# Optimization experiments

Hardware: AMD Instinct MI355X
Metric: run time of the kernel (lower is better)

The kernel has to match this reference:

```python
import jax, jax.numpy as jnp
import numpy as np

N_TOKEN = 267735
HEAD = 20000
CUTOFFS = [20000, 20008, 20016, 200000, 267735]  # from cl_root_leaf_dict with 2 roots of 8 leaves
N_ROOTS = 2


def setup_inputs() -> dict:
    key = jax.random.key(0)
    k1, k2, k3, k4 = jax.random.split(key, 4)
    N, D = 1024, 1024
    hidden = jax.random.normal(k1, (N, D), dtype=jnp.float32)
    target = jax.random.randint(k2, (N,), 0, N_TOKEN)
    W = jax.random.normal(k3, (N_TOKEN, D), dtype=jnp.float32) * 0.02
    b = jnp.zeros((N_TOKEN,), dtype=jnp.float32)
    cluster_weight = jax.random.normal(k4, (2, D), dtype=jnp.float32) * 0.02
    cluster_bias = jnp.zeros((2,), dtype=jnp.float32)
    return {"hidden": hidden, "target": target, "W": W, "b": b,
            "cluster_weight": cluster_weight, "cluster_bias": cluster_bias}


def _nll(hidden, target, W, b, cw, cb):
    cutoff_ends = [0] + CUTOFFS
    # head = first 20000 vocab rows + 2 cluster rows (d_proj == d_embed -> no projection)
    head_w = jnp.concatenate([W[:HEAD], cw], axis=0)          # [20002, D]
    head_b = jnp.concatenate([b[:HEAD], cb], axis=0)          # [20002]
    head_lp = jax.nn.log_softmax(hidden @ head_w.T + head_b, axis=-1)  # [N, 20002]
    n_head_cols = head_lp.shape[1]
    rows = jnp.arange(hidden.shape[0])
    # segment 0: target in [0, 20000) -> nll directly from head log-probs
    lp0 = head_lp[rows, jnp.clip(target, 0, HEAD - 1)]
    nll = -lp0  # only valid where target < HEAD; overwritten below otherwise
    for i in range(1, len(CUTOFFS)):
        l, r = cutoff_ends[i], cutoff_ends[i + 1]
        # per-segment tail logits for all tokens (masked combine keeps shapes static)
        tail_lp = jax.nn.log_softmax(hidden @ W[l:r].T + b[l:r], axis=-1)  # [N, r-l]
        # routing column exactly as in the torch code:
        # j = i-1 for root segments, -(i - n_roots) for the two cluster segments
        j = (i - 1) if i <= N_ROOTS else (n_head_cols - (i - N_ROOTS))
        lp_i = head_lp[:, j] + tail_lp[rows, jnp.clip(target - l, 0, r - l - 1)]
        mask = (target >= l) & (target < r)
        nll = jnp.where(mask, -lp_i, nll)
    return nll


def reference(hidden, target, W, b, cluster_weight, cluster_bias):
    return _nll(hidden, target, W, b, cluster_weight, cluster_bias)
```

## Files before the change

kernel.cpp:

```cpp
#include <hip/hip_runtime.h>
#include <hip/hip_bf16.h>

#define D_DIM 1024
#define NTOK 267735
#define NEXT_ 267737
#define HEADN 20000

typedef __attribute__((ext_vector_type(8))) short bf16x8;
typedef __attribute__((ext_vector_type(4))) float f32x4;

__device__ __forceinline__ int seg_of(int c){
  if (c < HEADN)  return 0;
  if (c < 20008)  return 1;
  if (c < 20016)  return 2;
  if (c < 200000) return 3;
  if (c < NTOK)   return 4;
  return 0;
}

__device__ __forceinline__ unsigned pack2(float x, float y){
  __hip_bfloat16 a = __float2bfloat16(x);
  __hip_bfloat16 b = __float2bfloat16(y);
  unsigned short ua = *reinterpret_cast<unsigned short*>(&a);
  unsigned short ub = *reinterpret_cast<unsigned short*>(&b);
  return (unsigned)ua | ((unsigned)ub << 16);
}

#define BM 256
#define BN 128
#define BK 32
#define LDP 40
#define NTHREADS 512

__global__ __launch_bounds__(NTHREADS, 1) void gemm_lse_kernel(
    const float* __restrict__ hidden, const float* __restrict__ W,
    const float* __restrict__ bias,   const float* __restrict__ cw,
    const float* __restrict__ cb,     float* __restrict__ accg)
{
  __shared__ unsigned short lsA[BM * LDP];
  __shared__ unsigned short lsB[BN * LDP];

  const int tid = threadIdx.x;
  const int rowBase = blockIdx.x * BM;
  const int colBase = blockIdx.y * BN;

  const float* aSrc[4]; int aRow[4], aK4[4];
#pragma unroll
  for (int i=0;i<4;++i){
    int idx = tid + NTHREADS*i;
    aRow[i] = idx >> 3; aK4[i] = idx & 7;
    aSrc[i] = hidden + (size_t)(rowBase + aRow[i]) * D_DIM + aK4[i]*4;
  }
  const float* bSrc[2]; int bRow[2], bK4[2];
#pragma unroll
  for (int i=0;i<2;++i){
    int idx = tid + NTHREADS*i;
    bRow[i] = idx >> 3; bK4[i] = idx & 7;
    int c = colBase + bRow[i];
    const float* base;
    if (c < NTOK)       base = W  + (size_t)c * D_DIM;
    else if (c < NEXT_) base = cw + (size_t)(c - NTOK) * D_DIM;
    else                base = W;
    bSrc[i] = base + bK4[i]*4;
  }

  const int lane = tid & 63;
  const int wv = tid >> 6;
  const int wm = wv >> 1;
  const int wn = wv & 1;

  f32x4 acc[4][4];
#pragma unroll
  for (int i=0;i<4;++i)
#pragma unroll
    for (int j=0;j<4;++j) acc[i][j] = (f32x4){0.f,0.f,0.f,0.f};

  const int aRd = (wm*64 + (lane&15)) * LDP + (lane>>4)*8;
  const int bRd = (wn*64 + (lane&15)) * LDP + (lane>>4)*8;

  for (int kt = 0; kt < D_DIM/BK; ++kt){
    float4 av[4], bv[2];
#pragma unroll
    for (int i=0;i<4;++i) av[i] = *reinterpret_cast<const float4*>(aSrc[i] + kt*BK);
#pragma unroll
    for (int i=0;i<2;++i) bv[i] = *reinterpret_cast<const float4*>(bSrc[i] + kt*BK);
    __syncthreads();
#pragma unroll
    for (int i=0;i<4;++i){
      unsigned* p = reinterpret_cast<unsigned*>(&lsA[aRow[i]*LDP + aK4[i]*4]);
      p[0] = pack2(av[i].x, av[i].y); p[1] = pack2(av[i].z, av[i].w);
    }
#pragma unroll
    for (int i=0;i<2;++i){
      unsigned* p = reinterpret_cast<unsigned*>(&lsB[bRow[i]*LDP + bK4[i]*4]);
      p[0] = pack2(bv[i].x, bv[i].y); p[1] = pack2(bv[i].z, bv[i].w);
    }
    __syncthreads();
    bf16x8 afr[4], bfr[4];
#pragma unroll
    for (int f=0; f<4; ++f) afr[f] = *reinterpret_cast<const bf16x8*>(&lsA[aRd + f*16*LDP]);
#pragma unroll
    for (int f=0; f<4; ++f) bfr[f] = *reinterpret_cast<const bf16x8*>(&lsB[bRd + f*16*LDP]);
#pragma unroll
    for (int i=0;i<4;++i)
#pragma unroll
      for (int j=0;j<4;++j)
        acc[i][j] = __builtin_amdgcn_mfma_f32_16x16x32_bf16(afr[i], bfr[j], acc[i][j], 0, 0, 0);
  }

  int sq[4]; float bq[4];
#pragma unroll
  for (int f=0; f<4; ++f){
    int c = colBase + wn*64 + f*16 + (lane & 15);
    if (c < NTOK)       { sq[f] = seg_of(c); bq[f] = bias[c]; }
    else if (c < NEXT_) { sq[f] = 0;         bq[f] = cb[c - NTOK]; }
    else                { sq[f] = -1;        bq[f] = 0.f; }
  }
  int sfirst = seg_of(colBase);
  int clast  = colBase + BN - 1; if (clast > NEXT_-1) clast = NEXT_-1;
  int slast  = seg_of(clast);
  int smin = sfirst, smax = slast;
  if (slast < sfirst){ smin = 0; smax = 4; }

#pragma unroll
  for (int i=0;i<4;++i){
#pragma unroll
    for (int r=0;r<4;++r){
      float e[4];
#pragma unroll
      for (int f=0;f<4;++f) e[f] = __expf(acc[i][f][r] + bq[f]);
      int rowg = rowBase + wm*64 + i*16 + (lane>>4)*4 + r;
      for (int s = smin; s <= smax; ++s){
        float p = 0.f;
#pragma unroll
        for (int f=0;f<4;++f) p += (sq[f]==s) ? e[f] : 0.f;
#pragma unroll
        for (int off=1; off<16; off<<=1) p += __shfl_xor(p, off, 16);
        if ((lane & 15) == 0 && p != 0.f) atomicAdd(&accg[rowg*8 + s], p);
      }
    }
  }
}

__global__ __launch_bounds__(256) void finalize_kernel(
    const float* __restrict__ hidden, const int* __restrict__ target,
    const float* __restrict__ W,      const float* __restrict__ bias,
    const float* __restrict__ cw,     const float* __restrict__ cb,
    const float* __restrict__ accg,   float* __restrict__ out)
{
  const int row  = blockIdx.x * 4 + (threadIdx.x >> 6);
  const int lane = threadIdx.x & 63;
  const int t = target[row];

  const float4* h4 = reinterpret_cast<const float4*>(hidden + (size_t)row * D_DIM);
  const float4* w1 = reinterpret_cast<const float4*>(W + (size_t)t * D_DIM);
  int s = 0; const float* jraw = W; float jb = 0.f;
  if (t >= HEADN){
    if      (t < 20008)  { s=1; jraw = W;          jb = bias[0]; }
    else if (t < 20016)  { s=2; jraw = W + D_DIM;  jb = bias[1]; }
    else if (t < 200000) { s=3; jraw = cw + D_DIM; jb = cb[1];   }
    else                 { s=4; jraw = cw;         jb = cb[0];   }
  }
  const float4* w2 = reinterpret_cast<const float4*>(jraw);

  float p1 = 0.f, p2 = 0.f;
#pragma unroll
  for (int j=0;j<4;++j){
    float4 hv = h4[lane + 64*j];
    float4 av = w1[lane + 64*j];
    float4 bv = w2[lane + 64*j];
    p1 += hv.x*av.x + hv.y*av.y + hv.z*av.z + hv.w*av.w;
    p2 += hv.x*bv.x + hv.y*bv.y + hv.z*bv.z + hv.w*bv.w;
  }
#pragma unroll
  for (int off=32; off; off>>=1){
    p1 += __shfl_xor(p1, off, 64);
    p2 += __shfl_xor(p2, off, 64);
  }

  if (lane == 0){
    float lseH = __logf(accg[row*8 + 0]);
    float nll;
    if (t < HEADN){
      nll = -(p1 + bias[t] - lseH);
    } else {
      float lseS = __logf(accg[row*8 + s]);
      nll = -((p2 + jb - lseH) + (p1 + bias[t] - lseS));
    }
    out[row] = nll;
  }
}

extern "C" void kernel_launch(void* const* d_in, const int* in_sizes, int n_in,
                              void* d_out, int out_size, void* d_ws, size_t ws_size,
                              hipStream_t stream)
{
  const float* hidden = (const float*)d_in[0];
  const int*   target = (const int*)  d_in[1];
  const float* W      = (const float*)d_in[2];
  const float* bias   = (const float*)d_in[3];
  const float* cw     = (const float*)d_in[4];
  const float* cb     = (const float*)d_in[5];
  float* out  = (float*)d_out;
  float* accg = (float*)d_ws;

  hipMemsetAsync(accg, 0, 1024*8*sizeof(float), stream);

  dim3 grid(1024/BM, (NEXT_ + BN - 1)/BN);
  gemm_lse_kernel<<<grid, NTHREADS, 0, stream>>>(hidden, W, bias, cw, cb, accg);
  finalize_kernel<<<256, 256, 0, stream>>>(hidden, target, W, bias, cw, cb, accg, out);
}
```

Baseline: 1.012 ms.

## Sort rows by target segment and skip unneeded tail GEMM tiles

A new prep kernel buckets the rows by the segment their target falls in, builds a permutation and per-segment row ranges, and zeroes the accumulators in place of the memset. The GEMM kernel reads hidden rows through this permutation and returns early for column tiles whose tail segment has no rows in the current row block, since those tail logsumexps are never used. It also replaces padded LDS rows with an XOR swizzle and prefetches the next k-slice into registers to overlap global loads with the MFMA work. The cost is an extra tiny single-block kernel launch and an indirect row gather.

Result: slower. 1.711 ms (+69.1%).

```diff
diff --git a/kernel.cpp b/kernel.cpp
--- a/kernel.cpp
+++ b/kernel.cpp
@@ -29,27 +29,72 @@
 #define BM 256
 #define BN 128
 #define BK 32
-#define LDP 40
 #define NTHREADS 512
+
+__global__ void prep_kernel(const int* __restrict__ target,
+                            float* __restrict__ accg,
+                            int* __restrict__ perm, int* __restrict__ segB)
+{
+  __shared__ int cnt[5]; __shared__ int base[5];
+  int t = threadIdx.x;
+  if (t < 5) cnt[t] = 0;
+  __syncthreads();
+  for (int i=0;i<8;++i) accg[t*8+i] = 0.f;
+  int s = seg_of(target[t]);
+  int pos = atomicAdd(&cnt[s], 1);
+  __syncthreads();
+  if (t == 0){
+    int acc = 0;
+    for (int q=0;q<5;++q){ base[q]=acc; segB[q*2]=acc; acc+=cnt[q]; segB[q*2+1]=acc; }
+  }
+  __syncthreads();
+  perm[base[s] + pos] = t;
+}
+
+__device__ __forceinline__ int swz_w(int r, int k4){
+  int c = (k4 >> 1) ^ ((r >> 1) & 3);
+  return r*32 + c*8 + (k4 & 1)*4;
+}
+__device__ __forceinline__ int swz_r(int row, int q){
+  return row*32 + ((q ^ ((row >> 1) & 3)) << 3);
+}
 
 __global__ __launch_bounds__(NTHREADS, 1) void gemm_lse_kernel(
     const float* __restrict__ hidden, const float* __restrict__ W,
     const float* __restrict__ bias,   const float* __restrict__ cw,
-    const float* __restrict__ cb,     float* __restrict__ accg)
-{
-  __shared__ unsigned short lsA[BM * LDP];
-  __shared__ unsigned short lsB[BN * LDP];
-
+    const float* __restrict__ cb,     float* __restrict__ accg,
+    const int* __restrict__ perm,     const int* __restrict__ segB)
+{
   const int tid = threadIdx.x;
   const int rowBase = blockIdx.x * BM;
   const int colBase = blockIdx.y * BN;
 
+  {
+    int cfirst = colBase;
+    int clast  = colBase + BN - 1; if (clast > NEXT_-1) clast = NEXT_-1;
+    bool need = (clast >= NTOK);
+    int clast2 = clast < NTOK ? clast : NTOK-1;
+    int sf = seg_of(cfirst), sl = seg_of(clast2);
+    for (int s = sf; s <= sl; ++s){
+      if (s == 0) { need = true; break; }
+      if (segB[2*s] < rowBase + BM && segB[2*s+1] > rowBase) need = true;
+    }
+    if (!need) return;
+  }
+
+  __shared__ unsigned short lsA[BM * 32];
+  __shared__ unsigned short lsB[BN * 32];
+  __shared__ int pperm[BM];
+
+  if (tid < BM) pperm[tid] = perm[rowBase + tid];
+  __syncthreads();
+
   const float* aSrc[4]; int aRow[4], aK4[4];
 #pragma unroll
   for (int i=0;i<4;++i){
     int idx = tid + NTHREADS*i;
     aRow[i] = idx >> 3; aK4[i] = idx & 7;
-    aSrc[i] = hidden + (size_t)(rowBase + aRow[i]) * D_DIM + aK4[i]*4;
+    aSrc[i] = hidden + (size_t)pperm[aRow[i]] * D_DIM + aK4[i]*4;
   }
   const float* bSrc[2]; int bRow[2], bK4[2];
 #pragma unroll
@@ -68,6 +113,8 @@
   const int wv = tid >> 6;
   const int wm = wv >> 1;
   const int wn = wv & 1;
+  const int q  = lane >> 4;
+  const int r16 = lane & 15;
 
   f32x4 acc[4][4];
 #pragma unroll
@@ -75,32 +122,36 @@
 #pragma unroll
     for (int j=0;j<4;++j) acc[i][j] = (f32x4){0.f,0.f,0.f,0.f};
 
-  const int aRd = (wm*64 + (lane&15)) * LDP + (lane>>4)*8;
-  const int bRd = (wn*64 + (lane&15)) * LDP + (lane>>4)*8;
+  float4 av[4], bv[2];
+#pragma unroll
+  for (int i=0;i<4;++i) av[i] = *reinterpret_cast<const float4*>(aSrc[i]);
+#pragma unroll
+  for (int i=0;i<2;++i) bv[i] = *reinterpret_cast<const float4*>(bSrc[i]);
 
   for (int kt = 0; kt < D_DIM/BK; ++kt){
-    float4 av[4], bv[2];
-#pragma unroll
-    for (int i=0;i<4;++i) av[i] = *reinterpret_cast<const float4*>(aSrc[i] + kt*BK);
-#pragma unroll
-    for (int i=0;i<2;++i) bv[i] = *reinterpret_cast<const float4*>(bSrc[i] + kt*BK);
     __syncthreads();
 #pragma unroll
     for (int i=0;i<4;++i){
-      unsigned* p = reinterpret_cast<unsigned*>(&lsA[aRow[i]*LDP + aK4[i]*4]);
+      unsigned* p = reinterpret_cast<unsigned*>(&lsA[swz_w(aRow[i], aK4[i])]);
       p[0] = pack2(av[i].x, av[i].y); p[1] = pack2(av[i].z, av[i].w);
     }
 #pragma unroll
     for (int i=0;i<2;++i){
-      unsigned* p = reinterpret_cast<unsigned*>(&lsB[bRow[i]*LDP + bK4[i]*4]);
+      unsigned* p = reinterpret_cast<unsigned*>(&lsB[swz_w(bRow[i], bK4[i])]);
       p[0] = pack2(bv[i].x, bv[i].y); p[1] = pack2(bv[i].z, bv[i].w);
     }
     __syncthreads();
+    if (kt + 1 < D_DIM/BK){
+#pragma unroll
+      for (int i=0;i<4;++i) av[i] = *reinterpret_cast<const float4*>(aSrc[i] + (kt+1)*BK);
+#pragma unroll
+      for (int i=0;i<2;++i) bv[i] = *reinterpret_cast<const float4*>(bSrc[i] + (kt+1)*BK);
+    }
     bf16x8 afr[4], bfr[4];
 #pragma unroll
-    for (int f=0; f<4; ++f) afr[f] = *reinterpret_cast<const bf16x8*>(&lsA[aRd + f*16*LDP]);
-#pragma unroll
-    for (int f=0; f<4; ++f) bfr[f] = *reinterpret_cast<const bf16x8*>(&lsB[bRd + f*16*LDP]);
+    for (int f=0; f<4; ++f) afr[f] = *reinterpret_cast<const bf16x8*>(&lsA[swz_r(wm*64 + f*16 + r16, q)]);
+#pragma unroll
+    for (int f=0; f<4; ++f) bfr[f] = *reinterpret_cast<const bf16x8*>(&lsB[swz_r(wn*64 + f*16 + r16, q)]);
 #pragma unroll
     for (int i=0;i<4;++i)
 #pragma unroll
@@ -111,7 +162,7 @@
   int sq[4]; float bq[4];
 #pragma unroll
   for (int f=0; f<4; ++f){
-    int c = colBase + wn*64 + f*16 + (lane & 15);
+    int c = colBase + wn*64 + f*16 + r16;
     if (c < NTOK)       { sq[f] = seg_of(c); bq[f] = bias[c]; }
     else if (c < NEXT_) { sq[f] = 0;         bq[f] = cb[c - NTOK]; }
     else                { sq[f] = -1;        bq[f] = 0.f; }
@@ -129,7 +180,7 @@
       float e[4];
 #pragma unroll
       for (int f=0;f<4;++f) e[f] = __expf(acc[i][f][r] + bq[f]);
-      int rowg = rowBase + wm*64 + i*16 + (lane>>4)*4 + r;
+      int rowg = pperm[wm*64 + i*16 + (lane>>4)*4 + r];
       for (int s = smin; s <= smax; ++s){
         float p = 0.f;
 #pragma unroll
@@ -203,10 +254,12 @@
   const float* cb     = (const float*)d_in[5];
   float* out  = (float*)d_out;
   float* accg = (float*)d_ws;
-
-  hipMemsetAsync(accg, 0, 1024*8*sizeof(float), stream);
+  int*   perm = (int*)((char*)d_ws + 32768);
+  int*   segB = (int*)((char*)d_ws + 36864);
+
+  prep_kernel<<<1, 1024, 0, stream>>>(target, accg, perm, segB);
 
   dim3 grid(1024/BM, (NEXT_ + BN - 1)/BN);
-  gemm_lse_kernel<<<grid, NTHREADS, 0, stream>>>(hidden, W, bias, cw, cb, accg);
+  gemm_lse_kernel<<<grid, NTHREADS, 0, stream>>>(hidden, W, bias, cw, cb, accg, perm, segB);
   finalize_kernel<<<256, 256, 0, stream>>>(hidden, target, W, bias, cw, cb, accg, out);
 }
```
